# Kernel optimization log

Measured on AMD Instinct MI355X. Metric: run time of the kernel, lower is better.

Reference implementation:

```python
import jax, jax.numpy as jnp
import numpy as np

B, F, H, N, S = 1024, 256, 256, 128, 2
DEV_MIN, DEV_MAX = 0.001, 0.01
LOG2PI = float(np.log(2.0 * np.pi))  # k/2*log(2pi) with k=2


def setup_inputs() -> dict:
    key = jax.random.key(0)
    ks = jax.random.split(key, 16)
    d = {}
    d['latents'] = jax.random.normal(ks[0], (B, F), jnp.float32)
    d['realPoints'] = jax.random.uniform(ks[1], (B, 2), jnp.float32)
    d['predMu'] = jax.random.uniform(ks[2], (B, 2), jnp.float32)
    d['predScale'] = 0.01 + 0.05 * jax.random.uniform(ks[3], (B, 2), jnp.float32)
    d['eps'] = jax.random.normal(ks[4], (S, B * N, 2), jnp.float32)
    dims = [F] + [H] * 5
    for i in range(5):
        d[f'W{i}'] = jax.random.normal(ks[5 + i], (dims[i], dims[i + 1]), jnp.float32) / np.sqrt(dims[i])
        d[f'b{i}'] = jnp.zeros((dims[i + 1],), jnp.float32)
    d['Wp'] = jax.random.normal(ks[10], (N, H, 2), jnp.float32) / np.sqrt(H)
    d['bp'] = jnp.zeros((N, 2), jnp.float32)
    return d


def _mvn_logprob(x, mu, s):
    # diagonal 2D Gaussian log_prob; broadcasts over leading dims
    z = (x - mu) / s
    return -0.5 * jnp.sum(z * z, axis=-1) - jnp.sum(jnp.log(s), axis=-1) - LOG2PI


def reference(latents, realPoints, predMu, predScale, eps,
              W0, b0, W1, b1, W2, b2, W3, b3, W4, b4, Wp, bp):
    h = latents
    for W, b in ((W0, b0), (W1, b1), (W2, b2), (W3, b3), (W4, b4)):
        h = jax.nn.relu(h @ W + b)
    mu = 0.5 + jnp.einsum('bh,nhk->bnk', h, Wp) + bp          # (B, N, 2)
    Bn, Nn = mu.shape[0], mu.shape[1]
    dev = jnp.linspace(DEV_MIN, DEV_MAX, Nn)[:, None]          # (N, 1)
    scale = jnp.tile(dev, (Bn, 2))                             # (B*N, 2)
    muF = mu.reshape(Bn * Nn, 2)

    # real-points loss: log_prob of each real point under all N gaussians, sigmoid
    pts_real = jnp.repeat(realPoints, Nn, axis=0)              # (B*N, 2)
    realLoss = jax.nn.sigmoid(_mvn_logprob(pts_real, muF, scale).reshape(Bn, Nn))

    # reparameterized samples: (S, B*N, 2) -> (S*N, B, 2)
    sampled = muF + scale * eps
    sampled = sampled.reshape(S, Bn, Nn, 2).transpose(0, 2, 1, 3).reshape(S * Nn, Bn, 2)

    # discriminator lossA: log_prob under detached predicted dist, sigmoid(-x), MSLE vs 0.5
    pmD = jax.lax.stop_gradient(predMu)
    psD = jax.lax.stop_gradient(predScale)
    la = _mvn_logprob(sampled, pmD, psD)                       # (S*N, B)
    la = la.reshape(S, Nn, Bn).transpose(2, 1, 0)              # (B, N, S)
    la = jax.nn.sigmoid(-la)
    lossA = jnp.mean(jnp.square(jnp.log1p(0.5) - jnp.log1p(la)), axis=-1)  # (B, N)

    # discriminator lossB: all-pairs log_prob of samples under own gaussians
    # equivalent to tf.repeat(sampled, N, axis=-2) then log_prob against (B*N,) batch
    z = (sampled[:, :, None, :] - mu[None, :, :, :]) / dev     # (S*N, B, N, 2)
    lb = -0.5 * jnp.sum(z * z, axis=-1) - 2.0 * jnp.log(dev[:, 0]) - LOG2PI  # (S*N, B, N)
    lb = lb.reshape(S, Nn, Bn, Nn).transpose(2, 1, 0, 3)       # (B, N, S, N)
    sm = jax.nn.softmax(lb, axis=-1)
    idx = jnp.arange(Nn)[None, :, None, None]
    diag = jnp.take_along_axis(sm, idx, axis=-1)[..., 0]       # (B, N, S)
    lossB = jnp.square(1.0 - diag)

    # generator loss: log_prob of detached samples under (non-detached) predicted dist
    gl = _mvn_logprob(jax.lax.stop_gradient(sampled), predMu, predScale)  # (S*N, B)
    gl = jax.nn.sigmoid(gl).reshape(S, Nn, Bn).transpose(2, 1, 0)
    gl = jnp.mean(gl, axis=-1)                                 # (B, N)
    genLoss = gl * jax.lax.stop_gradient(1.0 - realLoss)

    return (sampled, genLoss, realLoss, lossA, lossB)
```

## Files before the change

kernel.cpp:

```cpp
#include <hip/hip_runtime.h>
#include <math.h>

#define BB   1024
#define HH   256
#define NN   128
#define SS   2
#define RR   4
#define LOG2PI_F 1.8378770664093453f
#define DEV_MIN_F 0.001f
#define DEV_STEP_F 7.08661417322835e-05f
#define LOG1P_HALF 0.40546510810816438f
#define SHIFT_F 12.0f

#define OFF_GEN  524288
#define OFF_REAL 655360
#define OFF_A    786432
#define OFF_B    917504

typedef float f4_t __attribute__((ext_vector_type(4)));

#define FMA4(ACC, HS, WV)                                         \
    {                                                             \
        ACC.x = fmaf(HS, WV.x, ACC.x);                            \
        ACC.y = fmaf(HS, WV.y, ACC.y);                            \
        ACC.z = fmaf(HS, WV.z, ACC.z);                            \
        ACC.w = fmaf(HS, WV.w, ACC.w);                            \
    }

__global__ __launch_bounds__(256) void transpose_wp_kernel(
    const float* __restrict__ Wp, float* __restrict__ Wt) {
    const int k = blockIdx.x;
    const int j = threadIdx.x;
    Wt[k * 256 + j] = Wp[(j >> 1) * 512 + k * 2 + (j & 1)];
}

__global__ __launch_bounds__(1024, 4) void mlp_loss_kernel(
    const float* __restrict__ latents, const float* __restrict__ eps,
    const float* __restrict__ realPts, const float* __restrict__ predMu,
    const float* __restrict__ predScale,
    const float* __restrict__ W0, const float* __restrict__ b0,
    const float* __restrict__ W1, const float* __restrict__ b1,
    const float* __restrict__ W2, const float* __restrict__ b2,
    const float* __restrict__ W3, const float* __restrict__ b3,
    const float* __restrict__ W4, const float* __restrict__ b4,
    const float* __restrict__ Wt, const float* __restrict__ bp,
    float* __restrict__ out) {
    __shared__ __align__(16) float hb[RR][256];
    __shared__ __align__(16) float part[16][RR][256];
    __shared__ float2 sprm[NN];

    const int t  = threadIdx.x;
    const int q  = t >> 6;
    const int c  = t & 63;
    const int rL = t >> 8;
    const int j  = t & 255;
    const int brow = blockIdx.x * RR;

    if (t < NN) {
        float dv = DEV_MIN_F + (float)t * DEV_STEP_F;
        sprm[t] = make_float2(-0.5f / (dv * dv), -2.f * __logf(dv) - LOG2PI_F);
    }
    hb[rL][j] = latents[(brow + rL) * 256 + j];

    float biasv[6];
    biasv[0] = b0[j]; biasv[1] = b1[j]; biasv[2] = b2[j];
    biasv[3] = b3[j]; biasv[4] = b4[j]; biasv[5] = bp[j];

    const int nL = j >> 1, sL = j & 1;
    const int b = brow + rL;
    const float2 epv = ((const float2*)eps)[sL * (BB * NN) + b * NN + nL];

    __syncthreads();

    const float* Wsrc[6] = {W0, W1, W2, W3, W4, Wt};

    #pragma unroll
    for (int L = 0; L < 6; ++L) {
        const float* __restrict__ Wb = Wsrc[L] + (q * 16) * 256 + 4 * c;
        f4_t acc[4];
        #pragma unroll
        for (int r = 0; r < 4; ++r) acc[r] = (f4_t)0.f;

        #pragma unroll
        for (int i = 0; i < 4; ++i) {
            f4_t w0 = *(const f4_t*)(Wb + (i * 4 + 0) * 256);
            f4_t w1 = *(const f4_t*)(Wb + (i * 4 + 1) * 256);
            f4_t w2 = *(const f4_t*)(Wb + (i * 4 + 2) * 256);
            f4_t w3 = *(const f4_t*)(Wb + (i * 4 + 3) * 256);
            const int kb = q * 16 + i * 4;
            #pragma unroll
            for (int r = 0; r < 4; ++r) {
                f4_t hv = *(const f4_t*)&hb[r][kb];
                FMA4(acc[r], hv.x, w0);
                FMA4(acc[r], hv.y, w1);
                FMA4(acc[r], hv.z, w2);
                FMA4(acc[r], hv.w, w3);
            }
        }

        #pragma unroll
        for (int r = 0; r < 4; ++r)
            *(f4_t*)&part[q][r][4 * c] = acc[r];
        __syncthreads();

        float v0 = part[0][rL][j]  + part[1][rL][j]  + part[2][rL][j]  + part[3][rL][j];
        float v1 = part[4][rL][j]  + part[5][rL][j]  + part[6][rL][j]  + part[7][rL][j];
        float v2 = part[8][rL][j]  + part[9][rL][j]  + part[10][rL][j] + part[11][rL][j];
        float v3 = part[12][rL][j] + part[13][rL][j] + part[14][rL][j] + part[15][rL][j];
        float val = (v0 + v1) + (v2 + v3);
        val += biasv[L];
        if (L == 5) val += 0.5f;
        else        val = fmaxf(val, 0.f);
        hb[rL][j] = val;
        __syncthreads();
    }

    const float* __restrict__ muL = &hb[rL][0];
    const int n = nL, s = sL;
    const float devn = DEV_MIN_F + (float)n * DEV_STEP_F;
    const float2 prn = sprm[n];

    const float mux = muL[2 * n], muy = muL[2 * n + 1];
    const float px = fmaf(devn, epv.x, mux);
    const float py = fmaf(devn, epv.y, muy);

    ((float2*)out)[(size_t)(s * NN + n) * BB + b] = make_float2(px, py);

    const float2 pm = ((const float2*)predMu)[b];
    const float2 ps = ((const float2*)predScale)[b];
    const float2 rp = ((const float2*)realPts)[b];

    const int me = t & 3;
    float x1 = __shfl_xor(px, 1), y1 = __shfl_xor(py, 1);
    float x2 = __shfl_xor(px, 2), y2 = __shfl_xor(py, 2);
    float x3 = __shfl_xor(px, 3), y3 = __shfl_xor(py, 3);
    float PX0 = (me == 0) ? px : (me == 1) ? x1 : (me == 2) ? x2 : x3;
    float PY0 = (me == 0) ? py : (me == 1) ? y1 : (me == 2) ? y2 : y3;
    float PX1 = (me == 1) ? px : (me == 0) ? x1 : (me == 3) ? x2 : x3;
    float PY1 = (me == 1) ? py : (me == 0) ? y1 : (me == 3) ? y2 : y3;
    float PX2 = (me == 2) ? px : (me == 3) ? x1 : (me == 0) ? x2 : x3;
    float PY2 = (me == 2) ? py : (me == 3) ? y1 : (me == 0) ? y2 : y3;
    float PX3 = (me == 3) ? px : (me == 2) ? x1 : (me == 1) ? x2 : x3;
    float PY3 = (me == 3) ? py : (me == 2) ? y1 : (me == 1) ? y2 : y3;

    float S0 = 0.f, S1 = 0.f, S2 = 0.f, S3 = 0.f;
    #pragma unroll 4
    for (int mi = 0; mi < 16; ++mi) {
        f4_t mm = *(const f4_t*)&muL[16 * mi + 4 * me];
        f4_t pr = *(const f4_t*)((const float*)sprm + 16 * mi + 4 * me);
        float dx, dy, lb;
        dx = PX0 - mm.x; dy = PY0 - mm.y;
        lb = fmaf(fmaf(dx, dx, dy * dy), pr.x, pr.y); S0 += __expf(lb - SHIFT_F);
        dx = PX1 - mm.x; dy = PY1 - mm.y;
        lb = fmaf(fmaf(dx, dx, dy * dy), pr.x, pr.y); S1 += __expf(lb - SHIFT_F);
        dx = PX2 - mm.x; dy = PY2 - mm.y;
        lb = fmaf(fmaf(dx, dx, dy * dy), pr.x, pr.y); S2 += __expf(lb - SHIFT_F);
        dx = PX3 - mm.x; dy = PY3 - mm.y;
        lb = fmaf(fmaf(dx, dx, dy * dy), pr.x, pr.y); S3 += __expf(lb - SHIFT_F);
        dx = PX0 - mm.z; dy = PY0 - mm.w;
        lb = fmaf(fmaf(dx, dx, dy * dy), pr.z, pr.w); S0 += __expf(lb - SHIFT_F);
        dx = PX1 - mm.z; dy = PY1 - mm.w;
        lb = fmaf(fmaf(dx, dx, dy * dy), pr.z, pr.w); S1 += __expf(lb - SHIFT_F);
        dx = PX2 - mm.z; dy = PY2 - mm.w;
        lb = fmaf(fmaf(dx, dx, dy * dy), pr.z, pr.w); S2 += __expf(lb - SHIFT_F);
        dx = PX3 - mm.z; dy = PY3 - mm.w;
        lb = fmaf(fmaf(dx, dx, dy * dy), pr.z, pr.w); S3 += __expf(lb - SHIFT_F);
    }
    S0 += __shfl_xor(S0, 1); S1 += __shfl_xor(S1, 1);
    S2 += __shfl_xor(S2, 1); S3 += __shfl_xor(S3, 1);
    S0 += __shfl_xor(S0, 2); S1 += __shfl_xor(S1, 2);
    S2 += __shfl_xor(S2, 2); S3 += __shfl_xor(S3, 2);
    float sum = (me == 0) ? S0 : (me == 1) ? S1 : (me == 2) ? S2 : S3;

    float dxd = devn * epv.x, dyd = devn * epv.y;
    float lbd = fmaf(fmaf(dxd, dxd, dyd * dyd), prn.x, prn.y);
    float ed  = __expf(lbd - SHIFT_F);
    float diag = ed / sum;
    float lbv = (1.f - diag) * (1.f - diag);
    out[OFF_B + (size_t)b * (NN * SS) + j] = lbv;

    float zx = (px - pm.x) / ps.x, zy = (py - pm.y) / ps.y;
    float la = -0.5f * (zx * zx + zy * zy) - __logf(ps.x) - __logf(ps.y) - LOG2PI_F;
    float aa = 1.f / (1.f + __expf(la));
    float termA = LOG1P_HALF - log1pf(aa);
    termA = termA * termA;
    float gg = 1.f / (1.f + __expf(-la));

    float drx = rp.x - mux, dry = rp.y - muy;
    float lr = fmaf(fmaf(drx, drx, dry * dry), prn.x, prn.y);
    float rl = 1.f / (1.f + __expf(-lr));

    float termA_sum = termA + __shfl_xor(termA, 1);
    float gg_sum    = gg + __shfl_xor(gg, 1);
    if (s == 0) {
        out[OFF_GEN  + (size_t)b * NN + n] = 0.5f * gg_sum * (1.f - rl);
        out[OFF_REAL + (size_t)b * NN + n] = rl;
        out[OFF_A    + (size_t)b * NN + n] = 0.5f * termA_sum;
    }
}

extern "C" void kernel_launch(void* const* d_in, const int* in_sizes, int n_in,
                              void* d_out, int out_size, void* d_ws, size_t ws_size,
                              hipStream_t stream) {
    const float* latents   = (const float*)d_in[0];
    const float* realPts   = (const float*)d_in[1];
    const float* predMu    = (const float*)d_in[2];
    const float* predScale = (const float*)d_in[3];
    const float* eps       = (const float*)d_in[4];
    const float* W0 = (const float*)d_in[5];
    const float* b0 = (const float*)d_in[6];
    const float* W1 = (const float*)d_in[7];
    const float* b1 = (const float*)d_in[8];
    const float* W2 = (const float*)d_in[9];
    const float* b2 = (const float*)d_in[10];
    const float* W3 = (const float*)d_in[11];
    const float* b3 = (const float*)d_in[12];
    const float* W4 = (const float*)d_in[13];
    const float* b4 = (const float*)d_in[14];
    const float* Wp = (const float*)d_in[15];
    const float* bp = (const float*)d_in[16];

    float* Wtp = (float*)d_ws;

    transpose_wp_kernel<<<dim3(256), dim3(256), 0, stream>>>(Wp, Wtp);
    mlp_loss_kernel<<<dim3(BB / RR), dim3(1024), 0, stream>>>(
        latents, eps, realPts, predMu, predScale,
        W0, b0, W1, b1, W2, b2, W3, b3, W4, b4, Wtp, bp, (float*)d_out);
}
```

Measured before the change: 119.6 us.

## Prefetch next layer weights across LDS-only barriers and simplify shuffles

```diff
diff --git a/kernel.cpp b/kernel.cpp
--- a/kernel.cpp
+++ b/kernel.cpp
@@ -27,11 +27,15 @@
         ACC.w = fmaf(HS, WV.w, ACC.w);                            \
     }
 
+#define BAR_LGKM() asm volatile("s_waitcnt lgkmcnt(0)\n\ts_barrier" ::: "memory")
+
 __global__ __launch_bounds__(256) void transpose_wp_kernel(
     const float* __restrict__ Wp, float* __restrict__ Wt) {
-    const int k = blockIdx.x;
-    const int j = threadIdx.x;
-    Wt[k * 256 + j] = Wp[(j >> 1) * 512 + k * 2 + (j & 1)];
+    const int t = threadIdx.x;
+    const int k = blockIdx.x * 2 + (t >> 7);
+    const int n = t & 127;
+    const float2 v = ((const float2*)Wp)[n * 256 + k];
+    *(float2*)&Wt[k * 256 + 2 * n] = v;
 }
 
 __global__ __launch_bounds__(1024, 4) void mlp_loss_kernel(
@@ -70,19 +74,41 @@
     const int b = brow + rL;
     const float2 epv = ((const float2*)eps)[sL * (BB * NN) + b * NN + nL];
 
-    __syncthreads();
-
     const float* Wsrc[6] = {W0, W1, W2, W3, W4, Wt};
+    const int woff = (q * 16) * 256 + 4 * c;
+
+    f4_t wpa, wpb, wpc, wpd;
+    {
+        const float* Wn = W0 + woff;
+        wpa = *(const f4_t*)(Wn + 0 * 256);
+        wpb = *(const f4_t*)(Wn + 1 * 256);
+        wpc = *(const f4_t*)(Wn + 2 * 256);
+        wpd = *(const f4_t*)(Wn + 3 * 256);
+    }
+
+    BAR_LGKM();
 
     #pragma unroll
     for (int L = 0; L < 6; ++L) {
-        const float* __restrict__ Wb = Wsrc[L] + (q * 16) * 256 + 4 * c;
+        const float* __restrict__ Wb = Wsrc[L] + woff;
         f4_t acc[4];
         #pragma unroll
         for (int r = 0; r < 4; ++r) acc[r] = (f4_t)0.f;
 
+        {
+            const int kb = q * 16;
+            #pragma unroll
+            for (int r = 0; r < 4; ++r) {
+                f4_t hv = *(const f4_t*)&hb[r][kb];
+                FMA4(acc[r], hv.x, wpa);
+                FMA4(acc[r], hv.y, wpb);
+                FMA4(acc[r], hv.z, wpc);
+                FMA4(acc[r], hv.w, wpd);
+            }
+        }
+
         #pragma unroll
-        for (int i = 0; i < 4; ++i) {
+        for (int i = 1; i < 4; ++i) {
             f4_t w0 = *(const f4_t*)(Wb + (i * 4 + 0) * 256);
             f4_t w1 = *(const f4_t*)(Wb + (i * 4 + 1) * 256);
             f4_t w2 = *(const f4_t*)(Wb + (i * 4 + 2) * 256);
@@ -98,10 +124,18 @@
             }
         }
 
+        if (L < 5) {
+            const float* Wn = Wsrc[L + 1] + woff;
+            wpa = *(const f4_t*)(Wn + 0 * 256);
+            wpb = *(const f4_t*)(Wn + 1 * 256);
+            wpc = *(const f4_t*)(Wn + 2 * 256);
+            wpd = *(const f4_t*)(Wn + 3 * 256);
+        }
+
         #pragma unroll
         for (int r = 0; r < 4; ++r)
             *(f4_t*)&part[q][r][4 * c] = acc[r];
-        __syncthreads();
+        BAR_LGKM();
 
         float v0 = part[0][rL][j]  + part[1][rL][j]  + part[2][rL][j]  + part[3][rL][j];
         float v1 = part[4][rL][j]  + part[5][rL][j]  + part[6][rL][j]  + part[7][rL][j];
@@ -112,7 +146,7 @@
         if (L == 5) val += 0.5f;
         else        val = fmaxf(val, 0.f);
         hb[rL][j] = val;
-        __syncthreads();
+        BAR_LGKM();
     }
 
     const float* __restrict__ muL = &hb[rL][0];
@@ -130,19 +164,12 @@
     const float2 ps = ((const float2*)predScale)[b];
     const float2 rp = ((const float2*)realPts)[b];
 
+    float PX0 = px,              PY0 = py;
+    float PX1 = __shfl_xor(px, 1), PY1 = __shfl_xor(py, 1);
+    float PX2 = __shfl_xor(px, 2), PY2 = __shfl_xor(py, 2);
+    float PX3 = __shfl_xor(px, 3), PY3 = __shfl_xor(py, 3);
+
     const int me = t & 3;
-    float x1 = __shfl_xor(px, 1), y1 = __shfl_xor(py, 1);
-    float x2 = __shfl_xor(px, 2), y2 = __shfl_xor(py, 2);
-    float x3 = __shfl_xor(px, 3), y3 = __shfl_xor(py, 3);
-    float PX0 = (me == 0) ? px : (me == 1) ? x1 : (me == 2) ? x2 : x3;
-    float PY0 = (me == 0) ? py : (me == 1) ? y1 : (me == 2) ? y2 : y3;
-    float PX1 = (me == 1) ? px : (me == 0) ? x1 : (me == 3) ? x2 : x3;
-    float PY1 = (me == 1) ? py : (me == 0) ? y1 : (me == 3) ? y2 : y3;
-    float PX2 = (me == 2) ? px : (me == 3) ? x1 : (me == 0) ? x2 : x3;
-    float PY2 = (me == 2) ? py : (me == 3) ? y1 : (me == 0) ? y2 : y3;
-    float PX3 = (me == 3) ? px : (me == 2) ? x1 : (me == 1) ? x2 : x3;
-    float PY3 = (me == 3) ? py : (me == 2) ? y1 : (me == 1) ? y2 : y3;
-
     float S0 = 0.f, S1 = 0.f, S2 = 0.f, S3 = 0.f;
     #pragma unroll 4
     for (int mi = 0; mi < 16; ++mi) {
@@ -166,11 +193,8 @@
         dx = PX3 - mm.z; dy = PY3 - mm.w;
         lb = fmaf(fmaf(dx, dx, dy * dy), pr.z, pr.w); S3 += __expf(lb - SHIFT_F);
     }
-    S0 += __shfl_xor(S0, 1); S1 += __shfl_xor(S1, 1);
-    S2 += __shfl_xor(S2, 1); S3 += __shfl_xor(S3, 1);
-    S0 += __shfl_xor(S0, 2); S1 += __shfl_xor(S1, 2);
-    S2 += __shfl_xor(S2, 2); S3 += __shfl_xor(S3, 2);
-    float sum = (me == 0) ? S0 : (me == 1) ? S1 : (me == 2) ? S2 : S3;
+    float sum = S0 + __shfl_xor(S1, 1) + __shfl_xor(S2, 2) + __shfl_xor(S3, 3);
+    (void)me;
 
     float dxd = devn * epv.x, dyd = devn * epv.y;
     float lbd = fmaf(fmaf(dxd, dxd, dyd * dyd), prn.x, prn.y);
@@ -222,7 +246,7 @@
 
     float* Wtp = (float*)d_ws;
 
-    transpose_wp_kernel<<<dim3(256), dim3(256), 0, stream>>>(Wp, Wtp);
+    transpose_wp_kernel<<<dim3(128), dim3(256), 0, stream>>>(Wp, Wtp);
     mlp_loss_kernel<<<dim3(BB / RR), dim3(1024), 0, stream>>>(
         latents, eps, realPts, predMu, predScale,
         W0, b0, W1, b1, W2, b2, W3, b3, W4, b4, Wtp, bp, (float*)d_out);
```

Result: faster. 116.0 us (-3.0%).
